# Kernel tuning notes

Hardware: AMD Instinct MI355X
Metric: run time of the kernel (lower is better)

## Reference

```python
import jax, jax.numpy as jnp
import numpy as np

HEAD_SIZE = 64
N_EMBD = 1024
BLOCK_SIZE = 2048


def setup_inputs() -> dict:
    key = jax.random.key(0)
    ks = jax.random.split(key, 7)
    B, T = 4, 2048
    s = 1.0 / np.sqrt(N_EMBD)
    return {
        "x": jax.random.normal(ks[0], (B, T, N_EMBD), dtype=jnp.float32),
        "Wq": jax.random.normal(ks[1], (N_EMBD, HEAD_SIZE), dtype=jnp.float32) * s,
        "bq": jnp.zeros((HEAD_SIZE,), dtype=jnp.float32),
        "Wk": jax.random.normal(ks[2], (N_EMBD, HEAD_SIZE), dtype=jnp.float32) * s,
        "bk": jnp.zeros((HEAD_SIZE,), dtype=jnp.float32),
        "Wv": jax.random.normal(ks[3], (N_EMBD, HEAD_SIZE), dtype=jnp.float32) * s,
        "bv": jnp.zeros((HEAD_SIZE,), dtype=jnp.float32),
    }


def reference(x, Wq, bq, Wk, bk, Wv, bv):
    # x: [B, T, n_embd]
    B, T, _ = x.shape
    q = x @ Wq + bq  # [B, T, H]
    k = x @ Wk + bk
    v = x @ Wv + bv
    # Faithful to source: divides by head_size**(-0.5) == multiplies by sqrt(head_size)
    scale = jnp.float32(HEAD_SIZE) ** 0.5
    scores = jnp.einsum("bqh,bkh->bqk", q, k) * scale  # [B, T, T]
    causal = jnp.tril(jnp.ones((T, T), dtype=bool))
    scores = jnp.where(causal, scores, -jnp.inf)
    attn = jax.nn.softmax(scores, axis=-1)  # dropout p=0.0 (eval)
    out = jnp.einsum("bqk,bkh->bqh", attn, v)  # [B, T, H]
    return out
```

## Files before the change

kernel.cpp:

```cpp
#include <hip/hip_runtime.h>
#include <math.h>

#define NE 1024
#define HS 64
#define TT 2048
#define QSC 11.541560327111707f

typedef __bf16    v8bf __attribute__((ext_vector_type(8)));
typedef _Float16  v8h  __attribute__((ext_vector_type(8)));
typedef float     v4f  __attribute__((ext_vector_type(4)));

#define MFMA_BF(a, b, c)  __builtin_amdgcn_mfma_f32_16x16x32_bf16((a), (b), (c), 0, 0, 0)
#define MFMA_F16(a, b, c) __builtin_amdgcn_mfma_f32_16x16x32_f16((a), (b), (c), 0, 0, 0)

__device__ __forceinline__ void gl_lds16(const void* g, void* l) {
    __builtin_amdgcn_global_load_lds(
        (const __attribute__((address_space(1))) unsigned int*)g,
        (__attribute__((address_space(3))) unsigned int*)l, 16, 0, 0);
}
__device__ __forceinline__ void gl_lds4(const void* g, void* l) {
    __builtin_amdgcn_global_load_lds(
        (const __attribute__((address_space(1))) unsigned int*)g,
        (__attribute__((address_space(3))) unsigned int*)l, 4, 0, 0);
}

#define SYNC_VM(imm) do {                                   \
    __asm__ __volatile__("" ::: "memory");                  \
    __builtin_amdgcn_s_waitcnt(imm);                        \
    __builtin_amdgcn_s_barrier();                           \
    __asm__ __volatile__("" ::: "memory");                  \
} while (0)
#define WAIT_VM8  0x0F78
#define WAIT_VM0  0x0F70

__global__ __launch_bounds__(256) void prep_w(
    const float* __restrict__ Wq, const float* __restrict__ Wk,
    const float* __restrict__ Wv, char* __restrict__ imgW)
{
    __shared__ float t[64][65];
    const int bx = blockIdx.x, by = blockIdx.y;
    const float* W = (by == 0) ? Wq : ((by == 1) ? Wk : Wv);
    const int tid = threadIdx.x;
    const int cc = tid & 63, r4 = tid >> 6;
    #pragma unroll
    for (int p = 0; p < 16; ++p) {
        const int k = p * 4 + r4;
        t[k][cc] = W[(size_t)(bx * 64 + k) * HS + cc];
    }
    __syncthreads();
    #pragma unroll
    for (int e = 0; e < 4; ++e) {
        const int chunk = tid + e * 256;
        const int s2   = chunk >> 9;
        const int rem  = chunk & 511;
        const int ctl  = rem >> 7;
        const int rem2 = rem & 127;
        const int pl   = rem2 >> 6;
        const int rem3 = rem2 & 63;
        const int c    = rem3 >> 2;
        const int p16  = rem3 & 3;
        const int kb   = s2 * 32 + ((p16 ^ (c & 3)) << 3);
        const int ncol = ctl * 16 + c;
        v8bf o;
        #pragma unroll
        for (int j = 0; j < 8; ++j) {
            const float v = t[kb + j][ncol];
            const __bf16 h = (__bf16)v;
            o[j] = pl ? (__bf16)(v - (float)h) : h;
        }
        *(v8bf*)(imgW + (size_t)(bx * 2 + s2) * 24576
                 + (by * 4 + ctl) * 2048 + pl * 1024 + c * 64 + p16 * 16) = o;
    }
}

__global__ __launch_bounds__(256, 2) void proj(
    const float* __restrict__ x, const char* __restrict__ imgW,
    const float* __restrict__ bq, const float* __restrict__ bk,
    const float* __restrict__ bv,
    __bf16* __restrict__ qh, __bf16* __restrict__ ql,
    __bf16* __restrict__ kh, __bf16* __restrict__ kl,
    _Float16* __restrict__ vt)
{
    __shared__ __align__(16) char sbuf[3][26624];

    const int tid = threadIdx.x, lane = tid & 63, cg = tid >> 6;
    const int quad = lane >> 4, l16 = lane & 15;
    const int m0 = blockIdx.x * 16;

    const int wv = cg;
    const int xr0 = wv * 4 + (lane >> 5);
    const int xr1 = xr0 + 2;
    const int xp  = (lane >> 3) & 3;
    const int xj  = lane & 7;
    const float* gx0 = x + (size_t)(m0 + xr0) * NE + ((xp ^ (xr0 & 3)) << 3) + xj;
    const float* gx1 = x + (size_t)(m0 + xr1) * NE + ((xp ^ (xr1 & 3)) << 3) + xj;
    const int xl0 = wv * 512 + (lane & 63) * 4;
    const int xl1 = xl0 + 256;
    const char* gw = imgW + (size_t)tid * 16;

    v4f acc[3];
    #pragma unroll
    for (int i = 0; i < 3; ++i) acc[i] = (v4f){0.f, 0.f, 0.f, 0.f};

    #define STAGE(ks, xb_)  do {                                          \
        gl_lds4(gx0 + (ks) * 32, (xb_) + xl0);                            \
        gl_lds4(gx1 + (ks) * 32, (xb_) + xl1);                            \
        const char* gws_ = gw + (size_t)(ks) * 24576;                     \
        _Pragma("unroll")                                                 \
        for (int j_ = 0; j_ < 6; ++j_)                                    \
            gl_lds16(gws_ + j_ * 4096, (xb_) + 2048 + tid * 16 + j_ * 4096); \
    } while (0)

    auto compute = [&](int ks) {
        const char* xb = sbuf[ks % 3];
        const char* wb = xb + 2048;
        const int rl = l16;
        const int pA = quad ^ (rl & 3);
        const float4 a0 = *(const float4*)(xb + rl * 128 + pA * 32);
        const float4 a1 = *(const float4*)(xb + rl * 128 + pA * 32 + 16);
        const float av[8] = {a0.x, a0.y, a0.z, a0.w, a1.x, a1.y, a1.z, a1.w};
        v8bf ah, al;
        #pragma unroll
        for (int i = 0; i < 8; ++i) {
            const __bf16 h = (__bf16)av[i];
            ah[i] = h;
            al[i] = (__bf16)(av[i] - (float)h);
        }
        const int wo = l16 * 64 + ((quad ^ (l16 & 3)) << 4);
        #pragma unroll
        for (int j = 0; j < 3; ++j) {
            const char* base = wb + (cg * 3 + j) * 2048 + wo;
            const v8bf bh = *(const v8bf*)(base);
            const v8bf bl = *(const v8bf*)(base + 1024);
            acc[j] = MFMA_BF(ah, bh, acc[j]);
            acc[j] = MFMA_BF(ah, bl, acc[j]);
            acc[j] = MFMA_BF(al, bh, acc[j]);
        }
    };

    STAGE(0, sbuf[0]);
    STAGE(1, sbuf[1]);
    for (int ks = 0; ks < 31; ++ks) {
        SYNC_VM(WAIT_VM8);
        if (ks + 2 < 32) STAGE(ks + 2, sbuf[(ks + 2) % 3]);
        compute(ks);
    }
    SYNC_VM(WAIT_VM0);
    compute(31);
    #undef STAGE

    #pragma unroll
    for (int j = 0; j < 3; ++j) {
        const int n = cg * 48 + j * 16 + l16;
        const float bias = (n < 64) ? bq[n] : ((n < 128) ? bk[n - 64] : bv[n - 128]);
        #pragma unroll
        for (int reg = 0; reg < 4; ++reg) {
            const int row = m0 + quad * 4 + reg;
            const float v = acc[j][reg] + bias;
            if (n < 64) {
                const float s = v * QSC;
                const __bf16 hh = (__bf16)s;
                qh[(size_t)row * HS + n] = hh;
                ql[(size_t)row * HS + n] = (__bf16)(s - (float)hh);
            } else if (n < 128) {
                const __bf16 hh = (__bf16)v;
                kh[(size_t)row * HS + n - 64] = hh;
                kl[(size_t)row * HS + n - 64] = (__bf16)(v - (float)hh);
            } else {
                const int b2 = row >> 11, tt = row & 2047, hc = n - 128;
                vt[((size_t)(b2 * HS + hc)) * TT + tt] = (_Float16)v;
            }
        }
    }
}

__global__ __launch_bounds__(512, 2) void attn(
    const __bf16* __restrict__ qh, const __bf16* __restrict__ ql,
    const __bf16* __restrict__ kh, const __bf16* __restrict__ kl,
    const _Float16* __restrict__ vt, float* __restrict__ out)
{
    __shared__ __align__(16) char smem_raw[69632];
    _Float16* ps = (_Float16*)smem_raw;
    float*    os = (float*)smem_raw;
    __shared__ float sm[8][2][16], sl[8][2][16];

    const int tid = threadIdx.x, lane = tid & 63, w = tid >> 6;
    const int quad = lane >> 4, l16 = lane & 15;
    const int b = blockIdx.x & 3, pair = blockIdx.x >> 2;
    const int q0t[2] = {(127 - pair) * 16, pair * 16};
    const int ntk0 = (q0t[0] + 16 + 63) >> 6;
    const int ntk1 = (q0t[1] + 16 + 63) >> 6;
    const int total = ntk0 + ntk1;

    v8bf Qh0[2], Qh1[2], Ql0[2], Ql1[2];
    #pragma unroll
    for (int t = 0; t < 2; ++t) {
        const size_t qrow = ((size_t)b * TT + q0t[t] + l16) * HS;
        Qh0[t] = *(const v8bf*)(qh + qrow + quad * 8);
        Qh1[t] = *(const v8bf*)(qh + qrow + 32 + quad * 8);
        Ql0[t] = *(const v8bf*)(ql + qrow + quad * 8);
        Ql1[t] = *(const v8bf*)(ql + qrow + 32 + quad * 8);
    }

    const v8h vones = {(_Float16)1.f, (_Float16)1.f, (_Float16)1.f, (_Float16)1.f,
                       (_Float16)1.f, (_Float16)1.f, (_Float16)1.f, (_Float16)1.f};

    float mr0[4] = {-3e38f, -3e38f, -3e38f, -3e38f};
    float mr1[4] = {-3e38f, -3e38f, -3e38f, -3e38f};
    v4f o0[4], o1[4], l40, l41;
    #pragma unroll
    for (int i = 0; i < 4; ++i) {
        o0[i] = (v4f){0.f, 0.f, 0.f, 0.f};
        o1[i] = (v4f){0.f, 0.f, 0.f, 0.f};
    }
    l40 = (v4f){0.f, 0.f, 0.f, 0.f};
    l41 = (v4f){0.f, 0.f, 0.f, 0.f};

    _Float16* pw = ps + w * (16 * 72);

    auto doChunk = [&](int j0, int q0c, int t,
                       float (&mrow)[4], v4f (&o)[4], v4f &o4) {
        v8bf Kh[8], Kl[8];
        v8h  Vf[8];
        #pragma unroll
        for (int nt = 0; nt < 4; ++nt) {
            const size_t krow = ((size_t)b * TT + j0 + nt * 16 + l16) * HS;
            Kh[nt * 2]     = *(const v8bf*)(kh + krow + quad * 8);
            Kh[nt * 2 + 1] = *(const v8bf*)(kh + krow + 32 + quad * 8);
            Kl[nt * 2]     = *(const v8bf*)(kl + krow + quad * 8);
            Kl[nt * 2 + 1] = *(const v8bf*)(kl + krow + 32 + quad * 8);
        }
        #pragma unroll
        for (int nt = 0; nt < 4; ++nt) {
            const size_t vrow = ((size_t)(b * HS + nt * 16 + l16)) * TT + j0;
            Vf[nt * 2]     = *(const v8h*)(vt + vrow + quad * 8);
            Vf[nt * 2 + 1] = *(const v8h*)(vt + vrow + 32 + quad * 8);
        }
        v4f s[4];
        #pragma unroll
        for (int i = 0; i < 4; ++i) s[i] = (v4f){0.f, 0.f, 0.f, 0.f};
        #pragma unroll
        for (int nt = 0; nt < 4; ++nt) {
            s[nt] = MFMA_BF(Qh0[t], Kh[nt * 2],     s[nt]);
            s[nt] = MFMA_BF(Qh1[t], Kh[nt * 2 + 1], s[nt]);
            s[nt] = MFMA_BF(Qh0[t], Kl[nt * 2],     s[nt]);
            s[nt] = MFMA_BF(Qh1[t], Kl[nt * 2 + 1], s[nt]);
            s[nt] = MFMA_BF(Ql0[t], Kh[nt * 2],     s[nt]);
            s[nt] = MFMA_BF(Ql1[t], Kh[nt * 2 + 1], s[nt]);
        }
        const int irow = q0c + quad * 4;
        float mx[4] = {-3e38f, -3e38f, -3e38f, -3e38f};
        #pragma unroll
        for (int nt = 0; nt < 4; ++nt)
            #pragma unroll
            for (int reg = 0; reg < 4; ++reg) {
                if (j0 + nt * 16 + l16 > irow + reg) s[nt][reg] = -3e38f;
                mx[reg] = fmaxf(mx[reg], s[nt][reg]);
            }
        #pragma unroll
        for (int off = 8; off; off >>= 1)
            #pragma unroll
            for (int reg = 0; reg < 4; ++reg)
                mx[reg] = fmaxf(mx[reg], __shfl_xor(mx[reg], off));
        float al[4];
        #pragma unroll
        for (int reg = 0; reg < 4; ++reg) {
            const float mn = fmaxf(mrow[reg], mx[reg]);
            al[reg] = exp2f(mrow[reg] - mn);
            mrow[reg] = mn;
        }
        #pragma unroll
        for (int nt = 0; nt < 4; ++nt)
            #pragma unroll
            for (int reg = 0; reg < 4; ++reg) {
                const float p = (j0 + nt * 16 + l16 > irow + reg)
                                    ? 0.f : exp2f(s[nt][reg] - mrow[reg]);
                pw[(quad * 4 + reg) * 72 + nt * 16 + l16] = (_Float16)p;
            }
        #pragma unroll
        for (int nt = 0; nt < 4; ++nt)
            #pragma unroll
            for (int reg = 0; reg < 4; ++reg)
                o[nt][reg] *= al[reg];
        #pragma unroll
        for (int reg = 0; reg < 4; ++reg)
            o4[reg] *= al[reg];
        const v8h Pa0 = *(const v8h*)(pw + l16 * 72 + quad * 8);
        const v8h Pa1 = *(const v8h*)(pw + l16 * 72 + 32 + quad * 8);
        #pragma unroll
        for (int nt = 0; nt < 4; ++nt) {
            o[nt] = MFMA_F16(Pa0, Vf[nt * 2],     o[nt]);
            o[nt] = MFMA_F16(Pa1, Vf[nt * 2 + 1], o[nt]);
        }
        o4 = MFMA_F16(Pa0, vones, o4);
        o4 = MFMA_F16(Pa1, vones, o4);
    };

    for (int c = w; c < total; c += 8) {
        if (c < ntk0) doChunk(c * 64,          q0t[0], 0, mr0, o0, l40);
        else          doChunk((c - ntk0) * 64, q0t[1], 1, mr1, o1, l41);
    }

    if (l16 == 0) {
        #pragma unroll
        for (int reg = 0; reg < 4; ++reg) {
            sm[w][0][quad * 4 + reg] = mr0[reg];
            sl[w][0][quad * 4 + reg] = l40[reg];
            sm[w][1][quad * 4 + reg] = mr1[reg];
            sl[w][1][quad * 4 + reg] = l41[reg];
        }
    }
    __syncthreads();

    #pragma unroll
    for (int t = 0; t < 2; ++t) {
        float sc[4];
        #pragma unroll
        for (int reg = 0; reg < 4; ++reg) {
            const int r = quad * 4 + reg;
            float M = sm[0][t][r];
            #pragma unroll
            for (int i = 1; i < 8; ++i) M = fmaxf(M, sm[i][t][r]);
            const float mw = t ? mr1[reg] : mr0[reg];
            sc[reg] = exp2f(mw - M);
        }
        float* ow = os + (size_t)(w * 2 + t) * (16 * 68);
        #pragma unroll
        for (int nt = 0; nt < 4; ++nt)
            #pragma unroll
            for (int reg = 0; reg < 4; ++reg) {
                const v4f& oo = t ? o1[nt] : o0[nt];
                ow[(quad * 4 + reg) * 68 + nt * 16 + l16] = oo[reg] * sc[reg];
            }
    }
    __syncthreads();

    #pragma unroll
    for (int kk = 0; kk < 4; ++kk) {
        const int g = w * 4 + kk;
        const int t = g >> 4, m = g & 15;
        float M = sm[0][t][m];
        #pragma unroll
        for (int i = 1; i < 8; ++i) M = fmaxf(M, sm[i][t][m]);
        float L = 0.f, val = 0.f;
        #pragma unroll
        for (int i = 0; i < 8; ++i) {
            L   += sl[i][t][m] * exp2f(sm[i][t][m] - M);
            val += os[(size_t)(i * 2 + t) * (16 * 68) + m * 68 + lane];
        }
        out[((size_t)b * TT + q0t[t] + m) * HS + lane] = val / L;
    }
}

extern "C" void kernel_launch(void* const* d_in, const int* in_sizes, int n_in,
                              void* d_out, int out_size, void* d_ws, size_t ws_size,
                              hipStream_t stream)
{
    const float* x  = (const float*)d_in[0];
    const float* Wq = (const float*)d_in[1];
    const float* bq = (const float*)d_in[2];
    const float* Wk = (const float*)d_in[3];
    const float* bk = (const float*)d_in[4];
    const float* Wv = (const float*)d_in[5];
    const float* bv = (const float*)d_in[6];
    float* out = (float*)d_out;

    const int rows = in_sizes[0] / NE;
    char* p = (char*)d_ws;
    char* imgW = p;                           p += (size_t)32 * 24576;
    __bf16* qhb = (__bf16*)p;                 p += (size_t)rows * HS * 2;
    __bf16* qlb = (__bf16*)p;                 p += (size_t)rows * HS * 2;
    __bf16* khb = (__bf16*)p;                 p += (size_t)rows * HS * 2;
    __bf16* klb = (__bf16*)p;                 p += (size_t)rows * HS * 2;
    _Float16* vtb = (_Float16*)p;             p += (size_t)rows * HS * 2;

    prep_w<<<dim3(16, 3), 256, 0, stream>>>(Wq, Wk, Wv, imgW);
    proj<<<rows / 16, 256, 0, stream>>>(x, imgW, bq, bk, bv,
                                        qhb, qlb, khb, klb, vtb);
    attn<<<rows / 32, 512, 0, stream>>>(qhb, qlb, khb, klb, vtb, out);
}
```

Before: 136.4 us.

## Retile projection GEMM to 64-row blocks split across two column halves

The projection kernel now processes 64 rows per block with 512 threads, and a second grid dimension splits the 192 output columns into two halves of 96. This reduces how often each block re-reads the weight tiles relative to x. The x staging switches from 4-byte to 16-byte global-to-LDS loads, issued only by the first 256 threads. This lowers per-block weight traffic and LDS use, at the cost of half the threads idling during staging and a changed vmcnt wait threshold.

Measured after the change: 137.0 us. Within noise of the previous version (+0.4%).

```diff
diff --git a/kernel.cpp b/kernel.cpp
--- a/kernel.cpp
+++ b/kernel.cpp
@@ -17,11 +17,6 @@
     __builtin_amdgcn_global_load_lds(
         (const __attribute__((address_space(1))) unsigned int*)g,
         (__attribute__((address_space(3))) unsigned int*)l, 16, 0, 0);
-}
-__device__ __forceinline__ void gl_lds4(const void* g, void* l) {
-    __builtin_amdgcn_global_load_lds(
-        (const __attribute__((address_space(1))) unsigned int*)g,
-        (__attribute__((address_space(3))) unsigned int*)l, 4, 0, 0);
 }
 
 #define SYNC_VM(imm) do {                                   \
@@ -30,8 +25,8 @@
     __builtin_amdgcn_s_barrier();                           \
     __asm__ __volatile__("" ::: "memory");                  \
 } while (0)
-#define WAIT_VM8  0x0F78
-#define WAIT_VM0  0x0F70
+#define WAIT_VM5  0x0075
+#define WAIT_VM0  0x0070
 
 __global__ __launch_bounds__(256) void prep_w(
     const float* __restrict__ Wq, const float* __restrict__ Wk,
@@ -73,7 +68,7 @@
     }
 }
 
-__global__ __launch_bounds__(256, 2) void proj(
+__global__ __launch_bounds__(512, 2) void proj(
     const float* __restrict__ x, const char* __restrict__ imgW,
     const float* __restrict__ bq, const float* __restrict__ bk,
     const float* __restrict__ bv,
@@ -81,40 +76,42 @@
     __bf16* __restrict__ kh, __bf16* __restrict__ kl,
     _Float16* __restrict__ vt)
 {
-    __shared__ __align__(16) char sbuf[3][26624];
-
-    const int tid = threadIdx.x, lane = tid & 63, cg = tid >> 6;
+    __shared__ __align__(16) char sbuf[3][20480];
+
+    const int tid = threadIdx.x, lane = tid & 63, w = tid >> 6;
+    const int mt = w & 3, cg = w >> 2;
     const int quad = lane >> 4, l16 = lane & 15;
-    const int m0 = blockIdx.x * 16;
-
-    const int wv = cg;
-    const int xr0 = wv * 4 + (lane >> 5);
-    const int xr1 = xr0 + 2;
-    const int xp  = (lane >> 3) & 3;
-    const int xj  = lane & 7;
-    const float* gx0 = x + (size_t)(m0 + xr0) * NE + ((xp ^ (xr0 & 3)) << 3) + xj;
-    const float* gx1 = x + (size_t)(m0 + xr1) * NE + ((xp ^ (xr1 & 3)) << 3) + xj;
-    const int xl0 = wv * 512 + (lane & 63) * 4;
-    const int xl1 = xl0 + 256;
-    const char* gw = imgW + (size_t)tid * 16;
+    const int m0 = blockIdx.x * 64, n0 = blockIdx.y * 96;
+
+    const int xr0 = w * 16 + (lane >> 3);
+    const int xr1 = xr0 + 8;
+    const int xs  = lane & 7;
+    const float* gx0 = x + (size_t)(m0 + xr0) * NE
+                         + (((xs >> 1) ^ (xr0 & 3)) << 3) + (xs & 1) * 4;
+    const float* gx1 = x + (size_t)(m0 + xr1) * NE
+                         + (((xs >> 1) ^ (xr1 & 3)) << 3) + (xs & 1) * 4;
+    const char* gwb = imgW + n0 * 128 + w * 3072 + lane * 16;
 
     v4f acc[3];
     #pragma unroll
     for (int i = 0; i < 3; ++i) acc[i] = (v4f){0.f, 0.f, 0.f, 0.f};
 
-    #define STAGE(ks, xb_)  do {                                          \
-        gl_lds4(gx0 + (ks) * 32, (xb_) + xl0);                            \
-        gl_lds4(gx1 + (ks) * 32, (xb_) + xl1);                            \
-        const char* gws_ = gw + (size_t)(ks) * 24576;                     \
-        _Pragma("unroll")                                                 \
-        for (int j_ = 0; j_ < 6; ++j_)                                    \
-            gl_lds16(gws_ + j_ * 4096, (xb_) + 2048 + tid * 16 + j_ * 4096); \
+    #define STAGE(ks)  do {                                               \
+        if (tid < 256) {                                                  \
+            char* b_ = sbuf[(ks) % 3];                                    \
+            gl_lds16(gx0 + (ks) * 32, b_ + w * 2048 + lane * 16);         \
+            gl_lds16(gx1 + (ks) * 32, b_ + w * 2048 + 1024 + lane * 16);  \
+            const char* g_ = gwb + (size_t)(ks) * 24576;                  \
+            gl_lds16(g_,        b_ + 8192 + w * 3072 + lane * 16);        \
+            gl_lds16(g_ + 1024, b_ + 8192 + w * 3072 + 1024 + lane * 16); \
+            gl_lds16(g_ + 2048, b_ + 8192 + w * 3072 + 2048 + lane * 16); \
+        }                                                                 \
     } while (0)
 
     auto compute = [&](int ks) {
         const char* xb = sbuf[ks % 3];
-        const char* wb = xb + 2048;
-        const int rl = l16;
+        const char* wb = xb + 8192;
+        const int rl = mt * 16 + l16;
         const int pA = quad ^ (rl & 3);
         const float4 a0 = *(const float4*)(xb + rl * 128 + pA * 32);
         const float4 a1 = *(const float4*)(xb + rl * 128 + pA * 32 + 16);
@@ -138,11 +135,11 @@
         }
     };
 
-    STAGE(0, sbuf[0]);
-    STAGE(1, sbuf[1]);
+    STAGE(0);
+    STAGE(1);
     for (int ks = 0; ks < 31; ++ks) {
-        SYNC_VM(WAIT_VM8);
-        if (ks + 2 < 32) STAGE(ks + 2, sbuf[(ks + 2) % 3]);
+        SYNC_VM(WAIT_VM5);
+        if (ks + 2 < 32) STAGE(ks + 2);
         compute(ks);
     }
     SYNC_VM(WAIT_VM0);
@@ -151,11 +148,11 @@
 
     #pragma unroll
     for (int j = 0; j < 3; ++j) {
-        const int n = cg * 48 + j * 16 + l16;
+        const int n = n0 + (cg * 3 + j) * 16 + l16;
         const float bias = (n < 64) ? bq[n] : ((n < 128) ? bk[n - 64] : bv[n - 128]);
         #pragma unroll
         for (int reg = 0; reg < 4; ++reg) {
-            const int row = m0 + quad * 4 + reg;
+            const int row = m0 + mt * 16 + quad * 4 + reg;
             const float v = acc[j][reg] + bias;
             if (n < 64) {
                 const float s = v * QSC;
@@ -375,7 +372,7 @@
     _Float16* vtb = (_Float16*)p;             p += (size_t)rows * HS * 2;
 
     prep_w<<<dim3(16, 3), 256, 0, stream>>>(Wq, Wk, Wv, imgW);
-    proj<<<rows / 16, 256, 0, stream>>>(x, imgW, bq, bk, bv,
-                                        qhb, qlb, khb, klb, vtb);
+    proj<<<dim3(rows / 64, 2), 512, 0, stream>>>(x, imgW, bq, bk, bv,
+                                                 qhb, qlb, khb, klb, vtb);
     attn<<<rows / 32, 512, 0, stream>>>(qhb, qlb, khb, klb, vtb, out);
 }
```
